# Performance work log

Hardware: AMD Instinct MI355X
Metric: run time of the kernel (lower is better)

Reference implementation:

```python
import jax, jax.numpy as jnp
import numpy as np
from jax import lax

EPS = 1e-5
OUT_HW = 512  # origin image size for final bilinear upsample

def conv2d(x, w, pad, dil=1):
    # x: NCHW, w: OIHW
    return lax.conv_general_dilated(
        x, w, window_strides=(1, 1), padding=[(pad, pad), (pad, pad)],
        rhs_dilation=(dil, dil), dimension_numbers=('NCHW', 'OIHW', 'NCHW'))

def group_norm(x, gamma, beta, groups):
    B, C, H, W = x.shape
    xg = x.reshape(B, groups, C // groups, H, W)
    mu = jnp.mean(xg, axis=(2, 3, 4), keepdims=True)
    var = jnp.mean((xg - mu) ** 2, axis=(2, 3, 4), keepdims=True)
    xn = ((xg - mu) * lax.rsqrt(var + EPS)).reshape(B, C, H, W)
    return xn * gamma[None, :, None, None] + beta[None, :, None, None]

def mish(x):
    return x * jnp.tanh(jax.nn.softplus(x))

def setup_inputs() -> dict:
    key = jax.random.key(0)
    ks = jax.random.split(key, 8)
    s = 0.05  # keep conv outputs in a sane range
    return {
        'low_fea': jax.random.normal(ks[0], (48, 24, 128, 128), jnp.float32),
        'high_fea': jax.random.normal(ks[1], (48, 32, 128, 128), jnp.float32),
        'W_c0': jax.random.normal(ks[2], (16, 32, 1, 1), jnp.float32) * s,
        'W_c1': jax.random.normal(ks[3], (8, 8, 3, 3), jnp.float32) * s,
        'W_c2': jax.random.normal(ks[4], (8, 8, 3, 3), jnp.float32) * s,
        'g_bn': jnp.ones((16,), jnp.float32),
        'b_bn': jnp.zeros((16,), jnp.float32),
        'W_low': jax.random.normal(ks[5], (16, 24, 1, 1), jnp.float32) * s,
        'g_low': jnp.ones((16,), jnp.float32),
        'b_low': jnp.zeros((16,), jnp.float32),
        'W_ref': jax.random.normal(ks[6], (16, 16, 3, 3), jnp.float32) * s,
        'g_ref': jnp.ones((16,), jnp.float32),
        'b_ref': jnp.zeros((16,), jnp.float32),
        'W_seg': jax.random.normal(ks[7], (1, 16, 1, 1), jnp.float32) * s,
    }

def reference(low_fea, high_fea, W_c0, W_c1, W_c2, g_bn, b_bn,
              W_low, g_low, b_low, W_ref, g_ref, b_ref, W_seg):
    # DilatedParallelConvBlockD2(32, 16): 1x1 -> chunk -> (3x3 d1 | 3x3 d2) -> GN(1,16)
    in0 = conv2d(high_fea, W_c0, 0)            # [B,16,H,W]
    in1, in2 = in0[:, :8], in0[:, 8:]
    b1 = conv2d(in1, W_c1, 1, dil=1)
    b2 = conv2d(in2, W_c2, 2, dil=2)
    high = group_norm(jnp.concatenate([b1, b2], axis=1), g_bn, b_bn, groups=1)
    # up2_low 1x1 conv + GN(2,16)
    low = group_norm(conv2d(low_fea, W_low, 0), g_low, b_low, groups=2)
    # refine: Mish(high+low) -> 3x3 conv -> GN(2,16) -> Mish
    r = mish(high + low)
    r = mish(group_norm(conv2d(r, W_ref, 1), g_ref, b_ref, groups=2))
    # SegNIN 1x1 conv (dropout is identity at eval), bilinear upsample, sigmoid
    seg = conv2d(r, W_seg, 0)                  # [B,1,H,W]
    B = seg.shape[0]
    up = jax.image.resize(seg, (B, 1, OUT_HW, OUT_HW), method='bilinear')
    return jax.nn.sigmoid(up)
```

## Files before the change

kernel.cpp:

```cpp
#include <hip/hip_runtime.h>
#include <math.h>

#define BATCH 48
#define HH 128
#define WW 128
#define HW (128*128)
#define SZ (48*16*HW)
#define EPS 1e-5f

__device__ __forceinline__ float mishf(float v) {
    float t = __expf(fminf(v, 20.f));
    float u = t * (t + 2.f);
    return v * (u / (u + 2.f));
}

__device__ __forceinline__ void xcd_decode(int L, int bpb, int& b, int& w) {
    int xcd = L & 7;
    int j   = L >> 3;
    b = xcd + 8 * (j / bpb);
    w = j - (j / bpb) * bpb;
}

__global__ __launch_bounds__(256) void k_c0(const float* __restrict__ x,
                                            const float* __restrict__ W,
                                            const float* __restrict__ Wc1,
                                            const float* __restrict__ Wc2,
                                            const float* __restrict__ Wref,
                                            float* __restrict__ WTb,
                                            float* __restrict__ WTr,
                                            float* __restrict__ out) {
    __shared__ float w[16*32];
    int tid = threadIdx.x;
    for (int i = tid; i < 512; i += 256) w[i] = W[i];
    if (blockIdx.x == 0) {
        for (int i = tid; i < 576; i += 256) {
            int co = i & 7; int t = i >> 3; int kyx = t % 9; int ci = t / 9;
            WTb[(ci*9 + kyx)*8 + co]       = Wc1[(co*8 + ci)*9 + kyx];
            WTb[576 + (ci*9 + kyx)*8 + co] = Wc2[(co*8 + ci)*9 + kyx];
        }
        for (int i = tid; i < 2304; i += 256) {
            int co = i & 7; int t = i >> 3; int kyx = t % 9; int cih = t / 9;
            int ci = cih & 15; int h = cih >> 4;
            WTr[((h*16 + ci)*9 + kyx)*8 + co] = Wref[((h*8 + co)*16 + ci)*9 + kyx];
        }
    }
    __syncthreads();
    int b, wblk;
    xcd_decode(blockIdx.x, 16, b, wblk);
    int off = ((wblk*256 + tid) << 2);
    const float* xb = x + (size_t)b * 32 * HW + off;
    float acc[16][4];
    #pragma unroll
    for (int c = 0; c < 16; ++c) { acc[c][0]=acc[c][1]=acc[c][2]=acc[c][3]=0.f; }
    #pragma unroll 8
    for (int ci = 0; ci < 32; ++ci) {
        float4 xv = *(const float4*)(xb + (size_t)ci * HW);
        #pragma unroll
        for (int co = 0; co < 16; ++co) {
            float wv = w[co*32 + ci];
            acc[co][0] += wv*xv.x; acc[co][1] += wv*xv.y;
            acc[co][2] += wv*xv.z; acc[co][3] += wv*xv.w;
        }
    }
    float* ob = out + (size_t)b * 16 * HW + off;
    #pragma unroll
    for (int co = 0; co < 16; ++co)
        *(float4*)(ob + (size_t)co * HW) = make_float4(acc[co][0],acc[co][1],acc[co][2],acc[co][3]);
}

template<int D, int NCI>
__device__ __forceinline__ void dconv8(const float* __restrict__ base,
                                       const float* __restrict__ wb,
                                       const float* __restrict__ zb,
                                       float* __restrict__ obase,
                                       float* __restrict__ statp,
                                       int y0, int tid) {
    int tx = tid & 15, ty = tid >> 4;
    int y  = y0 + ty;
    int xg = tx*8 - 4;
    bool mx0 = (tx > 0);
    bool mx3 = (tx < 15);
    bool my[3];
    #pragma unroll
    for (int ky = 0; ky < 3; ++ky) my[ky] = ((unsigned)(y + D*(ky-1)) < 128u);

    float acc[8][8];
    #pragma unroll
    for (int c = 0; c < 8; ++c)
        #pragma unroll
        for (int j = 0; j < 8; ++j) acc[c][j] = 0.f;

    float4 A0,A1,A2,A3, B0,B1,B2,B3, C0,C1,C2,C3;

    auto LD = [&](const float* cb, int ky, float4& d0, float4& d1, float4& d2, float4& d3) {
        const float* rp = cb + (y + D*(ky-1))*WW;
        bool m = my[ky];
        d0 = *(const float4*)((m && mx0) ? rp      : zb);
        d1 = *(const float4*)( m         ? rp + 4  : zb);
        d2 = *(const float4*)( m         ? rp + 8  : zb);
        d3 = *(const float4*)((m && mx3) ? rp + 12 : zb);
    };
    auto FMAG = [&](const float* wp, float4 d0, float4 d1, float4 d2, float4 d3) {
        float u[16] = {d0.x,d0.y,d0.z,d0.w, d1.x,d1.y,d1.z,d1.w,
                       d2.x,d2.y,d2.z,d2.w, d3.x,d3.y,d3.z,d3.w};
        #pragma unroll
        for (int kx = 0; kx < 3; ++kx) {
            const float* wq = wp + kx*8;
            float w0 = wq[0], w1 = wq[1], w2 = wq[2], w3 = wq[3];
            float w4 = wq[4], w5 = wq[5], w6 = wq[6], w7 = wq[7];
            #pragma unroll
            for (int j = 0; j < 8; ++j) {
                float xv = u[4 - D + D*kx + j];
                acc[0][j] += w0*xv; acc[1][j] += w1*xv;
                acc[2][j] += w2*xv; acc[3][j] += w3*xv;
                acc[4][j] += w4*xv; acc[5][j] += w5*xv;
                acc[6][j] += w6*xv; acc[7][j] += w7*xv;
            }
        }
    };

    const float* cb = base + xg;
    const float* wp = wb;
    LD(cb, 0, A0,A1,A2,A3);
    #pragma unroll 1
    for (int ci = 0; ci < NCI; ++ci) {
        LD(cb, 1, B0,B1,B2,B3);
        FMAG(wp,      A0,A1,A2,A3);
        LD(cb, 2, C0,C1,C2,C3);
        FMAG(wp + 24, B0,B1,B2,B3);
        if (ci + 1 < NCI) LD(cb + HW, 0, A0,A1,A2,A3);
        FMAG(wp + 48, C0,C1,C2,C3);
        cb += HW; wp += 72;
    }

    float s = 0.f, q = 0.f;
    float* ob = obase + y*WW + tx*8;
    #pragma unroll
    for (int c = 0; c < 8; ++c) {
        *(float4*)(ob + (size_t)c*HW)     = make_float4(acc[c][0],acc[c][1],acc[c][2],acc[c][3]);
        *(float4*)(ob + (size_t)c*HW + 4) = make_float4(acc[c][4],acc[c][5],acc[c][6],acc[c][7]);
        #pragma unroll
        for (int j = 0; j < 8; ++j) { s += acc[c][j]; q += acc[c][j]*acc[c][j]; }
    }
    #pragma unroll
    for (int o = 32; o > 0; o >>= 1) { s += __shfl_down(s,o); q += __shfl_down(q,o); }
    if ((tid & 63) == 0) { atomicAdd(&statp[0], s); atomicAdd(&statp[1], q); }
}

__global__ __launch_bounds__(128) void k_branch4(const float* __restrict__ in0,
                                                 const float* __restrict__ WTb,
                                                 const float* __restrict__ zb,
                                                 float* __restrict__ outp,
                                                 float* __restrict__ stat) {
    int b, w;
    xcd_decode(blockIdx.x, 32, b, w);
    int br = w >> 4;
    int y0 = (w & 15) << 3;
    int tid = threadIdx.x;
    if (br == 0) {
        dconv8<1,8>(in0 + (size_t)(b*16    )*HW, WTb,       zb,
                    outp + (size_t)(b*16    )*HW, stat + b*2, y0, tid);
    } else {
        dconv8<2,8>(in0 + (size_t)(b*16 + 8)*HW, WTb + 576, zb,
                    outp + (size_t)(b*16 + 8)*HW, stat + b*2, y0, tid);
    }
}

__global__ __launch_bounds__(256) void k_low(const float* __restrict__ x,
                                             const float* __restrict__ W,
                                             float* __restrict__ outp,
                                             float* __restrict__ stat) {
    __shared__ float w[16*24];
    int tid = threadIdx.x;
    for (int i = tid; i < 384; i += 256) w[i] = W[i];
    __syncthreads();
    int b, wblk;
    xcd_decode(blockIdx.x, 16, b, wblk);
    int off = ((wblk*256 + tid) << 2);
    const float* xb = x + (size_t)b * 24 * HW + off;
    float acc[16][4];
    #pragma unroll
    for (int c = 0; c < 16; ++c) { acc[c][0]=acc[c][1]=acc[c][2]=acc[c][3]=0.f; }
    #pragma unroll 8
    for (int ci = 0; ci < 24; ++ci) {
        float4 xv = *(const float4*)(xb + (size_t)ci * HW);
        #pragma unroll
        for (int co = 0; co < 16; ++co) {
            float wv = w[co*24 + ci];
            acc[co][0] += wv*xv.x; acc[co][1] += wv*xv.y;
            acc[co][2] += wv*xv.z; acc[co][3] += wv*xv.w;
        }
    }
    float* ob = outp + (size_t)b * 16 * HW + off;
    float s0=0.f,q0=0.f,s1=0.f,q1=0.f;
    #pragma unroll
    for (int co = 0; co < 16; ++co) {
        *(float4*)(ob + (size_t)co * HW) = make_float4(acc[co][0],acc[co][1],acc[co][2],acc[co][3]);
        #pragma unroll
        for (int j = 0; j < 4; ++j) {
            if (co < 8) { s0 += acc[co][j]; q0 += acc[co][j]*acc[co][j]; }
            else        { s1 += acc[co][j]; q1 += acc[co][j]*acc[co][j]; }
        }
    }
    #pragma unroll
    for (int o = 32; o > 0; o >>= 1) {
        s0 += __shfl_down(s0,o); q0 += __shfl_down(q0,o);
        s1 += __shfl_down(s1,o); q1 += __shfl_down(q1,o);
    }
    if ((tid & 63) == 0) {
        atomicAdd(&stat[b*4+0], s0); atomicAdd(&stat[b*4+1], q0);
        atomicAdd(&stat[b*4+2], s1); atomicAdd(&stat[b*4+3], q1);
    }
}

__global__ __launch_bounds__(256) void k_fuse(const float* __restrict__ hp, const float* __restrict__ lp,
                                              const float* __restrict__ gbn, const float* __restrict__ bbn,
                                              const float* __restrict__ glow, const float* __restrict__ blow,
                                              const float* __restrict__ sh, const float* __restrict__ sl,
                                              float* __restrict__ r) {
    int b, wblk;
    xcd_decode(blockIdx.x, 256, b, wblk);
    int idx = wblk*256 + threadIdx.x;
    int p = b*262144 + (idx << 2);
    int c = idx >> 12;
    float muh = sh[b*2] * (1.f/262144.f);
    float varh = sh[b*2+1]*(1.f/262144.f) - muh*muh;
    float rsh = rsqrtf(varh + EPS);
    int gi = b*4 + (c>>3)*2;
    float mul = sl[gi] * (1.f/131072.f);
    float varl = sl[gi+1]*(1.f/131072.f) - mul*mul;
    float rsl = rsqrtf(varl + EPS);
    float ga = gbn[c]*rsh, bh = bbn[c] - muh*ga;
    float gl = glow[c]*rsl, bl = blow[c] - mul*gl;
    float4 h = *(const float4*)(hp + (size_t)p);
    float4 l = *(const float4*)(lp + (size_t)p);
    float4 o;
    o.x = mishf(h.x*ga + bh + l.x*gl + bl);
    o.y = mishf(h.y*ga + bh + l.y*gl + bl);
    o.z = mishf(h.z*ga + bh + l.z*gl + bl);
    o.w = mishf(h.w*ga + bh + l.w*gl + bl);
    *(float4*)(r + (size_t)p) = o;
}

__global__ __launch_bounds__(128) void k_ref4(const float* __restrict__ rin,
                                              const float* __restrict__ WTr,
                                              const float* __restrict__ zb,
                                              float* __restrict__ outp,
                                              float* __restrict__ stat) {
    int b, w;
    xcd_decode(blockIdx.x, 32, b, w);
    int h  = w >> 4;
    int y0 = (w & 15) << 3;
    int tid = threadIdx.x;
    dconv8<1,16>(rin + (size_t)b*16*HW, WTr + h*1152, zb,
                 outp + (size_t)(b*16 + h*8)*HW, stat + b*4 + h*2, y0, tid);
}

__global__ __launch_bounds__(256) void k_seg(const float* __restrict__ rp,
                                             const float* __restrict__ gref, const float* __restrict__ bref,
                                             const float* __restrict__ wseg, const float* __restrict__ sr,
                                             float* __restrict__ seg) {
    int b, wblk;
    xcd_decode(blockIdx.x, 16, b, wblk);
    int off = ((wblk*256 + threadIdx.x) << 2);
    const float* pb = rp + (size_t)b*16*HW + off;
    float ax=0.f, ay=0.f, az=0.f, aw=0.f;
    #pragma unroll
    for (int c = 0; c < 16; ++c) {
        int gi = b*4 + (c>>3)*2;
        float mu = sr[gi] * (1.f/131072.f);
        float var = sr[gi+1]*(1.f/131072.f) - mu*mu;
        float rs = rsqrtf(var + EPS);
        float ga = gref[c]*rs, bb = bref[c] - mu*ga;
        float wv = wseg[c];
        float4 v = *(const float4*)(pb + (size_t)c*HW);
        ax += wv*mishf(v.x*ga + bb);
        ay += wv*mishf(v.y*ga + bb);
        az += wv*mishf(v.z*ga + bb);
        aw += wv*mishf(v.w*ga + bb);
    }
    *(float4*)(seg + (size_t)b*HW + off) = make_float4(ax,ay,az,aw);
}

__global__ __launch_bounds__(256) void k_up(const float* __restrict__ seg, float* __restrict__ out) {
    int i4 = blockIdx.x * 256 + threadIdx.x;
    int b = i4 / (512*128);
    int rem = i4 - b*(512*128);
    int y = rem >> 7; int k = rem & 127;
    const float* sp = seg + (size_t)b * HW;
    float fy = fminf(fmaxf(0.25f*y - 0.375f, 0.f), 127.f);
    int y0 = min((int)fy, 126);
    float wy = fy - (float)y0;
    const float* r0 = sp + y0*WW;
    const float* r1 = r0 + WW;
    float res[4];
    #pragma unroll
    for (int j = 0; j < 4; ++j) {
        int x = k*4 + j;
        float fx = fminf(fmaxf(0.25f*x - 0.375f, 0.f), 127.f);
        int x0 = min((int)fx, 126);
        float wx = fx - (float)x0;
        float v0 = r0[x0]*(1.f-wx) + r0[x0+1]*wx;
        float v1 = r1[x0]*(1.f-wx) + r1[x0+1]*wx;
        float v = v0*(1.f-wy) + v1*wy;
        res[j] = 1.f/(1.f + __expf(-v));
    }
    *(float4*)(out + (size_t)i4*4) = make_float4(res[0],res[1],res[2],res[3]);
}

extern "C" void kernel_launch(void* const* d_in, const int* in_sizes, int n_in,
                              void* d_out, int out_size, void* d_ws, size_t ws_size,
                              hipStream_t stream) {
    const float* low  = (const float*)d_in[0];
    const float* high = (const float*)d_in[1];
    const float* Wc0  = (const float*)d_in[2];
    const float* Wc1  = (const float*)d_in[3];
    const float* Wc2  = (const float*)d_in[4];
    const float* gbn  = (const float*)d_in[5];
    const float* bbn  = (const float*)d_in[6];
    const float* Wlow = (const float*)d_in[7];
    const float* glow = (const float*)d_in[8];
    const float* blow = (const float*)d_in[9];
    const float* Wref = (const float*)d_in[10];
    const float* gref = (const float*)d_in[11];
    const float* bref = (const float*)d_in[12];
    const float* Wseg = (const float*)d_in[13];

    float* ws = (float*)d_ws;
    float* A  = ws;
    float* Bb = ws + (size_t)SZ;
    float* C  = ws + 2*(size_t)SZ;
    float* D  = ws + 3*(size_t)SZ;
    float* ST = D + (size_t)48*HW;
    float* ZB = ST + 480;
    float* WTb = ZB + 64;
    float* WTr = WTb + 1152;

    hipMemsetAsync(ST, 0, (480 + 64)*sizeof(float), stream);

    k_c0     <<<768,   256, 0, stream>>>(high, Wc0, Wc1, Wc2, Wref, WTb, WTr, A);
    k_branch4<<<1536,  128, 0, stream>>>(A, WTb, ZB, Bb, ST);
    k_low    <<<768,   256, 0, stream>>>(low, Wlow, C, ST + 96);
    k_fuse   <<<12288, 256, 0, stream>>>(Bb, C, gbn, bbn, glow, blow, ST, ST + 96, A);
    k_ref4   <<<1536,  128, 0, stream>>>(A, WTr, ZB, Bb, ST + 288);
    k_seg    <<<768,   256, 0, stream>>>(Bb, gref, bref, Wseg, ST + 288, D);
    k_up     <<<12288, 256, 0, stream>>>(D, (float*)d_out);
}
```

Baseline: 433.8 us.

## Store intermediate activations in fp16 to halve workspace traffic

All intermediate tensors (1x1 conv output, branch conv outputs, low-path conv, fused Mish map, refine conv output, seg map) are written and read as fp16, while arithmetic and statistics stay in fp32. The fuse and seg kernels now process 8 elements per thread, with their grid sizes halved to match. This targets the memory-bandwidth cost of the intermediate round-trips between kernels. The trade is reduced precision in the intermediates, which may affect accuracy against the fp32 reference.

```diff
diff --git a/kernel.cpp b/kernel.cpp
--- a/kernel.cpp
+++ b/kernel.cpp
@@ -1,4 +1,5 @@
 #include <hip/hip_runtime.h>
+#include <hip/hip_fp16.h>
 #include <math.h>
 
 #define BATCH 48
@@ -7,6 +8,17 @@
 #define HW (128*128)
 #define SZ (48*16*HW)
 #define EPS 1e-5f
+
+struct __align__(8)  h4 { __half2 a, b; };
+struct __align__(16) h8 { __half2 a, b, c, d; };
+
+__device__ __forceinline__ float4 h4f(h4 v) {
+    float2 f0 = __half22float2(v.a), f1 = __half22float2(v.b);
+    return make_float4(f0.x, f0.y, f1.x, f1.y);
+}
+__device__ __forceinline__ h4 f4h(float4 v) {
+    h4 r; r.a = __floats2half2_rn(v.x, v.y); r.b = __floats2half2_rn(v.z, v.w); return r;
+}
 
 __device__ __forceinline__ float mishf(float v) {
     float t = __expf(fminf(v, 20.f));
@@ -28,7 +40,7 @@
                                             const float* __restrict__ Wref,
                                             float* __restrict__ WTb,
                                             float* __restrict__ WTr,
-                                            float* __restrict__ out) {
+                                            __half* __restrict__ out) {
     __shared__ float w[16*32];
     int tid = threadIdx.x;
     for (int i = tid; i < 512; i += 256) w[i] = W[i];
@@ -62,17 +74,17 @@
             acc[co][2] += wv*xv.z; acc[co][3] += wv*xv.w;
         }
     }
-    float* ob = out + (size_t)b * 16 * HW + off;
+    __half* ob = out + (size_t)b * 16 * HW + off;
     #pragma unroll
     for (int co = 0; co < 16; ++co)
-        *(float4*)(ob + (size_t)co * HW) = make_float4(acc[co][0],acc[co][1],acc[co][2],acc[co][3]);
+        *(h4*)(ob + (size_t)co * HW) = f4h(make_float4(acc[co][0],acc[co][1],acc[co][2],acc[co][3]));
 }
 
 template<int D, int NCI>
-__device__ __forceinline__ void dconv8(const float* __restrict__ base,
+__device__ __forceinline__ void dconv8(const __half* __restrict__ base,
                                        const float* __restrict__ wb,
-                                       const float* __restrict__ zb,
-                                       float* __restrict__ obase,
+                                       const __half* __restrict__ zh,
+                                       __half* __restrict__ obase,
                                        float* __restrict__ statp,
                                        int y0, int tid) {
     int tx = tid & 15, ty = tid >> 4;
@@ -90,19 +102,20 @@
         #pragma unroll
         for (int j = 0; j < 8; ++j) acc[c][j] = 0.f;
 
-    float4 A0,A1,A2,A3, B0,B1,B2,B3, C0,C1,C2,C3;
-
-    auto LD = [&](const float* cb, int ky, float4& d0, float4& d1, float4& d2, float4& d3) {
-        const float* rp = cb + (y + D*(ky-1))*WW;
+    h4 A0,A1,A2,A3, B0,B1,B2,B3, C0,C1,C2,C3;
+
+    auto LD = [&](const __half* cb, int ky, h4& d0, h4& d1, h4& d2, h4& d3) {
+        const __half* rp = cb + (y + D*(ky-1))*WW;
         bool m = my[ky];
-        d0 = *(const float4*)((m && mx0) ? rp      : zb);
-        d1 = *(const float4*)( m         ? rp + 4  : zb);
-        d2 = *(const float4*)( m         ? rp + 8  : zb);
-        d3 = *(const float4*)((m && mx3) ? rp + 12 : zb);
+        d0 = *(const h4*)((m && mx0) ? rp      : zh);
+        d1 = *(const h4*)( m         ? rp + 4  : zh);
+        d2 = *(const h4*)( m         ? rp + 8  : zh);
+        d3 = *(const h4*)((m && mx3) ? rp + 12 : zh);
     };
-    auto FMAG = [&](const float* wp, float4 d0, float4 d1, float4 d2, float4 d3) {
-        float u[16] = {d0.x,d0.y,d0.z,d0.w, d1.x,d1.y,d1.z,d1.w,
-                       d2.x,d2.y,d2.z,d2.w, d3.x,d3.y,d3.z,d3.w};
+    auto FMAG = [&](const float* wp, h4 d0, h4 d1, h4 d2, h4 d3) {
+        float4 f0 = h4f(d0), f1 = h4f(d1), f2 = h4f(d2), f3 = h4f(d3);
+        float u[16] = {f0.x,f0.y,f0.z,f0.w, f1.x,f1.y,f1.z,f1.w,
+                       f2.x,f2.y,f2.z,f2.w, f3.x,f3.y,f3.z,f3.w};
         #pragma unroll
         for (int kx = 0; kx < 3; ++kx) {
             const float* wq = wp + kx*8;
@@ -119,7 +132,7 @@
         }
     };
 
-    const float* cb = base + xg;
+    const __half* cb = base + xg;
     const float* wp = wb;
     LD(cb, 0, A0,A1,A2,A3);
     #pragma unroll 1
@@ -134,11 +147,15 @@
     }
 
     float s = 0.f, q = 0.f;
-    float* ob = obase + y*WW + tx*8;
+    __half* ob = obase + y*WW + tx*8;
     #pragma unroll
     for (int c = 0; c < 8; ++c) {
-        *(float4*)(ob + (size_t)c*HW)     = make_float4(acc[c][0],acc[c][1],acc[c][2],acc[c][3]);
-        *(float4*)(ob + (size_t)c*HW + 4) = make_float4(acc[c][4],acc[c][5],acc[c][6],acc[c][7]);
+        h8 o;
+        o.a = __floats2half2_rn(acc[c][0], acc[c][1]);
+        o.b = __floats2half2_rn(acc[c][2], acc[c][3]);
+        o.c = __floats2half2_rn(acc[c][4], acc[c][5]);
+        o.d = __floats2half2_rn(acc[c][6], acc[c][7]);
+        *(h8*)(ob + (size_t)c*HW) = o;
         #pragma unroll
         for (int j = 0; j < 8; ++j) { s += acc[c][j]; q += acc[c][j]*acc[c][j]; }
     }
@@ -147,10 +164,10 @@
     if ((tid & 63) == 0) { atomicAdd(&statp[0], s); atomicAdd(&statp[1], q); }
 }
 
-__global__ __launch_bounds__(128) void k_branch4(const float* __restrict__ in0,
+__global__ __launch_bounds__(128) void k_branch5(const __half* __restrict__ in0,
                                                  const float* __restrict__ WTb,
-                                                 const float* __restrict__ zb,
-                                                 float* __restrict__ outp,
+                                                 const __half* __restrict__ zh,
+                                                 __half* __restrict__ outp,
                                                  float* __restrict__ stat) {
     int b, w;
     xcd_decode(blockIdx.x, 32, b, w);
@@ -158,17 +175,17 @@
     int y0 = (w & 15) << 3;
     int tid = threadIdx.x;
     if (br == 0) {
-        dconv8<1,8>(in0 + (size_t)(b*16    )*HW, WTb,       zb,
+        dconv8<1,8>(in0 + (size_t)(b*16    )*HW, WTb,       zh,
                     outp + (size_t)(b*16    )*HW, stat + b*2, y0, tid);
     } else {
-        dconv8<2,8>(in0 + (size_t)(b*16 + 8)*HW, WTb + 576, zb,
+        dconv8<2,8>(in0 + (size_t)(b*16 + 8)*HW, WTb + 576, zh,
                     outp + (size_t)(b*16 + 8)*HW, stat + b*2, y0, tid);
     }
 }
 
 __global__ __launch_bounds__(256) void k_low(const float* __restrict__ x,
                                              const float* __restrict__ W,
-                                             float* __restrict__ outp,
+                                             __half* __restrict__ outp,
                                              float* __restrict__ stat) {
     __shared__ float w[16*24];
     int tid = threadIdx.x;
@@ -191,11 +208,11 @@
             acc[co][2] += wv*xv.z; acc[co][3] += wv*xv.w;
         }
     }
-    float* ob = outp + (size_t)b * 16 * HW + off;
+    __half* ob = outp + (size_t)b * 16 * HW + off;
     float s0=0.f,q0=0.f,s1=0.f,q1=0.f;
     #pragma unroll
     for (int co = 0; co < 16; ++co) {
-        *(float4*)(ob + (size_t)co * HW) = make_float4(acc[co][0],acc[co][1],acc[co][2],acc[co][3]);
+        *(h4*)(ob + (size_t)co * HW) = f4h(make_float4(acc[co][0],acc[co][1],acc[co][2],acc[co][3]));
         #pragma unroll
         for (int j = 0; j < 4; ++j) {
             if (co < 8) { s0 += acc[co][j]; q0 += acc[co][j]*acc[co][j]; }
@@ -213,16 +230,16 @@
     }
 }
 
-__global__ __launch_bounds__(256) void k_fuse(const float* __restrict__ hp, const float* __restrict__ lp,
+__global__ __launch_bounds__(256) void k_fuse(const __half* __restrict__ hp, const __half* __restrict__ lp,
                                               const float* __restrict__ gbn, const float* __restrict__ bbn,
                                               const float* __restrict__ glow, const float* __restrict__ blow,
                                               const float* __restrict__ sh, const float* __restrict__ sl,
-                                              float* __restrict__ r) {
+                                              __half* __restrict__ r) {
     int b, wblk;
-    xcd_decode(blockIdx.x, 256, b, wblk);
+    xcd_decode(blockIdx.x, 128, b, wblk);
     int idx = wblk*256 + threadIdx.x;
-    int p = b*262144 + (idx << 2);
-    int c = idx >> 12;
+    int p = b*262144 + (idx << 3);
+    int c = idx >> 11;
     float muh = sh[b*2] * (1.f/262144.f);
     float varh = sh[b*2+1]*(1.f/262144.f) - muh*muh;
     float rsh = rsqrtf(varh + EPS);
@@ -232,39 +249,49 @@
     float rsl = rsqrtf(varl + EPS);
     float ga = gbn[c]*rsh, bh = bbn[c] - muh*ga;
     float gl = glow[c]*rsl, bl = blow[c] - mul*gl;
-    float4 h = *(const float4*)(hp + (size_t)p);
-    float4 l = *(const float4*)(lp + (size_t)p);
-    float4 o;
-    o.x = mishf(h.x*ga + bh + l.x*gl + bl);
-    o.y = mishf(h.y*ga + bh + l.y*gl + bl);
-    o.z = mishf(h.z*ga + bh + l.z*gl + bl);
-    o.w = mishf(h.w*ga + bh + l.w*gl + bl);
-    *(float4*)(r + (size_t)p) = o;
-}
-
-__global__ __launch_bounds__(128) void k_ref4(const float* __restrict__ rin,
+    h8 hv = *(const h8*)(hp + (size_t)p);
+    h8 lv = *(const h8*)(lp + (size_t)p);
+    float2 h01 = __half22float2(hv.a), h23 = __half22float2(hv.b),
+           h45 = __half22float2(hv.c), h67 = __half22float2(hv.d);
+    float2 l01 = __half22float2(lv.a), l23 = __half22float2(lv.b),
+           l45 = __half22float2(lv.c), l67 = __half22float2(lv.d);
+    float o0 = mishf(h01.x*ga + bh + l01.x*gl + bl);
+    float o1 = mishf(h01.y*ga + bh + l01.y*gl + bl);
+    float o2 = mishf(h23.x*ga + bh + l23.x*gl + bl);
+    float o3 = mishf(h23.y*ga + bh + l23.y*gl + bl);
+    float o4 = mishf(h45.x*ga + bh + l45.x*gl + bl);
+    float o5 = mishf(h45.y*ga + bh + l45.y*gl + bl);
+    float o6 = mishf(h67.x*ga + bh + l67.x*gl + bl);
+    float o7 = mishf(h67.y*ga + bh + l67.y*gl + bl);
+    h8 ov;
+    ov.a = __floats2half2_rn(o0,o1); ov.b = __floats2half2_rn(o2,o3);
+    ov.c = __floats2half2_rn(o4,o5); ov.d = __floats2half2_rn(o6,o7);
+    *(h8*)(r + (size_t)p) = ov;
+}
+
+__global__ __launch_bounds__(128) void k_ref5(const __half* __restrict__ rin,
                                               const float* __restrict__ WTr,
-                                              const float* __restrict__ zb,
-                                              float* __restrict__ outp,
+                                              const __half* __restrict__ zh,
+                                              __half* __restrict__ outp,
                                               float* __restrict__ stat) {
     int b, w;
     xcd_decode(blockIdx.x, 32, b, w);
     int h  = w >> 4;
     int y0 = (w & 15) << 3;
     int tid = threadIdx.x;
-    dconv8<1,16>(rin + (size_t)b*16*HW, WTr + h*1152, zb,
+    dconv8<1,16>(rin + (size_t)b*16*HW, WTr + h*1152, zh,
                  outp + (size_t)(b*16 + h*8)*HW, stat + b*4 + h*2, y0, tid);
 }
 
-__global__ __launch_bounds__(256) void k_seg(const float* __restrict__ rp,
+__global__ __launch_bounds__(256) void k_seg(const __half* __restrict__ rp,
                                              const float* __restrict__ gref, const float* __restrict__ bref,
                                              const float* __restrict__ wseg, const float* __restrict__ sr,
-                                             float* __restrict__ seg) {
+                                             __half* __restrict__ seg) {
     int b, wblk;
-    xcd_decode(blockIdx.x, 16, b, wblk);
-    int off = ((wblk*256 + threadIdx.x) << 2);
-    const float* pb = rp + (size_t)b*16*HW + off;
-    float ax=0.f, ay=0.f, az=0.f, aw=0.f;
+    xcd_decode(blockIdx.x, 8, b, wblk);
+    int off = ((wblk*256 + threadIdx.x) << 3);
+    const __half* pb = rp + (size_t)b*16*HW + off;
+    float a0=0,a1=0,a2=0,a3=0,a4=0,a5=0,a6=0,a7=0;
     #pragma unroll
     for (int c = 0; c < 16; ++c) {
         int gi = b*4 + (c>>3)*2;
@@ -273,26 +300,31 @@
         float rs = rsqrtf(var + EPS);
         float ga = gref[c]*rs, bb = bref[c] - mu*ga;
         float wv = wseg[c];
-        float4 v = *(const float4*)(pb + (size_t)c*HW);
-        ax += wv*mishf(v.x*ga + bb);
-        ay += wv*mishf(v.y*ga + bb);
-        az += wv*mishf(v.z*ga + bb);
-        aw += wv*mishf(v.w*ga + bb);
-    }
-    *(float4*)(seg + (size_t)b*HW + off) = make_float4(ax,ay,az,aw);
-}
-
-__global__ __launch_bounds__(256) void k_up(const float* __restrict__ seg, float* __restrict__ out) {
+        h8 v = *(const h8*)(pb + (size_t)c*HW);
+        float2 v01 = __half22float2(v.a), v23 = __half22float2(v.b),
+               v45 = __half22float2(v.c), v67 = __half22float2(v.d);
+        a0 += wv*mishf(v01.x*ga + bb); a1 += wv*mishf(v01.y*ga + bb);
+        a2 += wv*mishf(v23.x*ga + bb); a3 += wv*mishf(v23.y*ga + bb);
+        a4 += wv*mishf(v45.x*ga + bb); a5 += wv*mishf(v45.y*ga + bb);
+        a6 += wv*mishf(v67.x*ga + bb); a7 += wv*mishf(v67.y*ga + bb);
+    }
+    h8 ov;
+    ov.a = __floats2half2_rn(a0,a1); ov.b = __floats2half2_rn(a2,a3);
+    ov.c = __floats2half2_rn(a4,a5); ov.d = __floats2half2_rn(a6,a7);
+    *(h8*)(seg + (size_t)b*HW + off) = ov;
+}
+
+__global__ __launch_bounds__(256) void k_up(const __half* __restrict__ seg, float* __restrict__ out) {
     int i4 = blockIdx.x * 256 + threadIdx.x;
     int b = i4 / (512*128);
     int rem = i4 - b*(512*128);
     int y = rem >> 7; int k = rem & 127;
-    const float* sp = seg + (size_t)b * HW;
+    const __half* sp = seg + (size_t)b * HW;
     float fy = fminf(fmaxf(0.25f*y - 0.375f, 0.f), 127.f);
     int y0 = min((int)fy, 126);
     float wy = fy - (float)y0;
-    const float* r0 = sp + y0*WW;
-    const float* r1 = r0 + WW;
+    const __half* r0 = sp + y0*WW;
+    const __half* r1 = r0 + WW;
     float res[4];
     #pragma unroll
     for (int j = 0; j < 4; ++j) {
@@ -300,8 +332,8 @@
         float fx = fminf(fmaxf(0.25f*x - 0.375f, 0.f), 127.f);
         int x0 = min((int)fx, 126);
         float wx = fx - (float)x0;
-        float v0 = r0[x0]*(1.f-wx) + r0[x0+1]*wx;
-        float v1 = r1[x0]*(1.f-wx) + r1[x0+1]*wx;
+        float v0 = __half2float(r0[x0])*(1.f-wx) + __half2float(r0[x0+1])*wx;
+        float v1 = __half2float(r1[x0])*(1.f-wx) + __half2float(r1[x0+1])*wx;
         float v = v0*(1.f-wy) + v1*wy;
         res[j] = 1.f/(1.f + __expf(-v));
     }
@@ -327,11 +359,11 @@
     const float* Wseg = (const float*)d_in[13];
 
     float* ws = (float*)d_ws;
-    float* A  = ws;
-    float* Bb = ws + (size_t)SZ;
-    float* C  = ws + 2*(size_t)SZ;
-    float* D  = ws + 3*(size_t)SZ;
-    float* ST = D + (size_t)48*HW;
+    __half* A  = (__half*)ws;
+    __half* Bb = (__half*)(ws + (size_t)SZ);
+    __half* C  = (__half*)(ws + 2*(size_t)SZ);
+    __half* D  = (__half*)(ws + 3*(size_t)SZ);
+    float* ST = ws + 3*(size_t)SZ + (size_t)48*HW;
     float* ZB = ST + 480;
     float* WTb = ZB + 64;
     float* WTr = WTb + 1152;
@@ -339,10 +371,10 @@
     hipMemsetAsync(ST, 0, (480 + 64)*sizeof(float), stream);
 
     k_c0     <<<768,   256, 0, stream>>>(high, Wc0, Wc1, Wc2, Wref, WTb, WTr, A);
-    k_branch4<<<1536,  128, 0, stream>>>(A, WTb, ZB, Bb, ST);
+    k_branch5<<<1536,  128, 0, stream>>>(A, WTb, (const __half*)ZB, Bb, ST);
     k_low    <<<768,   256, 0, stream>>>(low, Wlow, C, ST + 96);
-    k_fuse   <<<12288, 256, 0, stream>>>(Bb, C, gbn, bbn, glow, blow, ST, ST + 96, A);
-    k_ref4   <<<1536,  128, 0, stream>>>(A, WTr, ZB, Bb, ST + 288);
-    k_seg    <<<768,   256, 0, stream>>>(Bb, gref, bref, Wseg, ST + 288, D);
+    k_fuse   <<<6144,  256, 0, stream>>>(Bb, C, gbn, bbn, glow, blow, ST, ST + 96, A);
+    k_ref5   <<<1536,  128, 0, stream>>>(A, WTr, (const __half*)ZB, Bb, ST + 288);
+    k_seg    <<<384,   256, 0, stream>>>(Bb, gref, bref, Wseg, ST + 288, D);
     k_up     <<<12288, 256, 0, stream>>>(D, (float*)d_out);
 }
```

Result: faster. 417.0 us (-3.9%).
